# Kernel tuning notes

Measured on AMD Instinct MI355X. Metric: run time of the kernel, lower is better.

Reference implementation:

```python
import jax, jax.numpy as jnp
import numpy as np

B, T, S, D = 32, 1024, 1024, 512
VOCAB = 1000
INSERT_TOK = jnp.array([1, 2], dtype=jnp.int64)


def setup_inputs() -> dict:
    key = jax.random.key(0)
    k1, k2, k3, k4, k5 = jax.random.split(key, 5)
    input_var = jax.random.randint(k1, (B, T), 0, VOCAB, dtype=jnp.int64)
    output = jax.random.normal(k2, (B, T, D), jnp.float32)
    context = jax.random.normal(k3, (B, S, D), jnp.float32)
    # nn.Linear(2*dim, dim): weight [D, 2D], bias [D]
    W = jax.random.normal(k4, (D, 2 * D), jnp.float32) / np.sqrt(2 * D)
    b = jax.random.normal(k5, (D,), jnp.float32) * 0.01
    return {"input_var": input_var, "output": output, "context": context,
            "di": 0, "W": W, "b": b}


def _hard_align(input_var, src_len):
    """Replicates the python double-loop: sequential 'inserted' counter per batch.
    Returns (j, valid): j[b,i] = column of the 1.0 in attn row i (torch negative
    indices wrapped), valid[b,i] = whether row i gets any 1.0 at all."""
    bsz, tgt_len = input_var.shape
    flags = jnp.isin(input_var, INSERT_TOK)  # [B,T] is token an insert token

    def step(inserted, xi):
        i, flag = xi  # i: scalar position, flag: [B]
        cond = (src_len >= i - inserted)                    # gate, per batch
        ins2 = inserted + jnp.where(cond & flag, 1, 0)      # increment before write
        j = i - ins2 - 1
        j = jnp.where(j < 0, j + src_len, j)                # torch negative-index wrap
        return ins2, (j, cond)

    idxs = jnp.arange(1, tgt_len, dtype=jnp.int32)
    init = jnp.zeros((bsz,), jnp.int32)  # init_inserted()
    _, (j_rows, valid) = jax.lax.scan(step, init, (idxs, flags[:, 1:].T))
    j_rows = j_rows.T      # [B,T-1]
    valid = valid.T        # [B,T-1]
    # row 0: attn[b,0,0] = 1.0 always
    j_full = jnp.concatenate([jnp.zeros((bsz, 1), j_rows.dtype), j_rows], axis=1)
    valid_full = jnp.concatenate([jnp.ones((bsz, 1), bool), valid], axis=1)
    return j_full, valid_full


def reference(input_var, output, context, di, W, b):
    bsz, tgt_len, hid = output.shape
    src_len = context.shape[1]
    j, valid = _hard_align(input_var, src_len)              # [B,T], [B,T]
    vf = valid[:, :, None].astype(output.dtype)
    # hard one-hot attention matrix (as the module materializes it)
    attn = jax.nn.one_hot(j, src_len, dtype=output.dtype) * vf  # [B,T,S]
    # mix = bmm(attn, context) == masked gather of context rows
    mix = jnp.take_along_axis(context, j[:, :, None].astype(jnp.int32), axis=1) * vf
    combined = jnp.concatenate([mix, output], axis=-1)      # [B,T,2D]
    out = jnp.tanh(combined @ W.T + b)                      # [B,T,D]
    return out, attn
```

## Files before the change

kernel.cpp:

```cpp
#include <hip/hip_runtime.h>
#include <hip/hip_bf16.h>

#define B_ 32
#define T_ 1024
#define S_ 1024
#define D_ 512
#define M_ (B_*T_)
#define N_ D_
#define K_ (2*D_)

typedef __attribute__((ext_vector_type(8))) short bf16x8;
typedef __attribute__((ext_vector_type(4))) float f32x4;

__device__ inline unsigned short f2bf(float x) {
    union { float f; unsigned u; } v; v.f = x;
    unsigned r = v.u + 0x7FFFu + ((v.u >> 16) & 1u);
    return (unsigned short)(r >> 16);
}

__device__ inline unsigned cvt2bf(float lo, float hi) {
#if __has_builtin(__builtin_amdgcn_cvt_pk_bf16_f32)
    typedef __attribute__((ext_vector_type(2))) __bf16 bf2;
    union { bf2 v; unsigned u; } r;
    r.v = __builtin_amdgcn_cvt_pk_bf16_f32(lo, hi);
    return r.u;
#else
    return (unsigned)f2bf(lo) | ((unsigned)f2bf(hi) << 16);
#endif
}

__device__ inline float fast_tanh(float x) {
#if __has_builtin(__builtin_amdgcn_exp2f) && __has_builtin(__builtin_amdgcn_rcpf)
    const float e = __builtin_amdgcn_exp2f(x * 2.885390082f);
    const float r = __builtin_amdgcn_rcpf(e + 1.0f);
    return 1.0f - 2.0f * r;
#else
    return tanhf(x);
#endif
}

__global__ void align_kernel(const int* __restrict__ iv, int* __restrict__ jbuf) {
    const int b = blockIdx.x;
    const int lane = threadIdx.x;
    const int* row = iv + b * T_;
    int f[16];
    int local = 0;
    const int t0 = lane * 16;
    #pragma unroll
    for (int q = 0; q < 16; ++q) {
        const int t = t0 + q;
        const int tok = row[t];
        const int fl = (t > 0 && (tok == 1 || tok == 2)) ? 1 : 0;
        f[q] = fl;
        local += fl;
    }
    int incl = local;
    #pragma unroll
    for (int off = 1; off < 64; off <<= 1) {
        const int up = __shfl_up(incl, off, 64);
        if (lane >= off) incl += up;
    }
    int run = incl - local;
    #pragma unroll
    for (int q = 0; q < 16; ++q) {
        const int t = t0 + q;
        run += f[q];
        int j;
        if (t == 0) {
            j = 0;
        } else {
            j = t - run - 1;
            if (j < 0) j += S_;
        }
        jbuf[b * T_ + t] = j;
    }
}

__global__ void pack_w(const float* __restrict__ W, unsigned short* __restrict__ Wbf) {
    const int idx = blockIdx.x * blockDim.x + threadIdx.x;
    const f32x4 a = ((const f32x4*)W)[idx * 2];
    const f32x4 c = ((const f32x4*)W)[idx * 2 + 1];
    union { bf16x8 v; unsigned u[4]; } pk;
    pk.u[0] = cvt2bf(a[0], a[1]); pk.u[1] = cvt2bf(a[2], a[3]);
    pk.u[2] = cvt2bf(c[0], c[1]); pk.u[3] = cvt2bf(c[2], c[3]);
    *(bf16x8*)(Wbf + (size_t)idx * 8) = pk.v;
}

#define BM 128
#define BN 128
#define BK 64
#define KMAX (K_ - BK)
#define NGEMM ((M_ / BM) * (N_ / BN))
#define NATTN 512

__global__ __launch_bounds__(256, 3)
void gemm_attn(const unsigned short* __restrict__ Wbf,
               const float* __restrict__ bias,
               float* __restrict__ out,
               float* __restrict__ attn,
               const float* __restrict__ ctx,
               const float* __restrict__ outp,
               const int* __restrict__ jbuf) {
    const int bx = blockIdx.x;
    const int tid = threadIdx.x;

    if (bx < NATTN) {
        const int m0 = bx * 64;
        #pragma unroll 4
        for (int r = 0; r < 64; ++r) {
            const int row = m0 + r;
            const int j = jbuf[row];
            f32x4 v = {0.f, 0.f, 0.f, 0.f};
            if ((j >> 2) == tid) v[j & 3] = 1.0f;
            ((f32x4*)(attn + (size_t)row * S_))[tid] = v;
        }
        return;
    }

    __shared__ unsigned short As[BM * BK];
    __shared__ unsigned short Bs[BN * BK];

    const int gbx  = bx - NATTN;
    const int lane = tid & 63;
    const int wave = tid >> 6;
    const int wm = wave >> 1, wn = wave & 1;
    const int l16 = lane & 15, quad = lane >> 4;

    const int xcd = gbx & 7;
    const int bn  = (gbx >> 3) & 3;
    const int bm  = ((gbx >> 5) << 3) | xcd;
    const int mBase = bm * BM;
    const int nBase = bn * BN;

    const int kc   = tid & 7;
    const int rsub = tid >> 3;
    const int sw   = kc ^ (rsub & 7);
    const float* actx[4];
    const float* aout[4];
    #pragma unroll
    for (int it = 0; it < 4; ++it) {
        const int r = it * 32 + rsub;
        const int m = mBase + r;
        const int jm = jbuf[m];
        actx[it] = ctx + ((size_t)((m >> 10) * S_ + jm)) * D_ + kc * 8;
        aout[it] = outp + (size_t)m * D_ - D_ + kc * 8;
    }

    f32x4 acc[4][4] = {};
    f32x4 fa[4][2];

#define LOAD_A(KO) do {                                                        \
    const int _koa = (KO);                                                     \
    _Pragma("unroll")                                                          \
    for (int _it = 0; _it < 4; ++_it) {                                        \
        const float* _src = (_koa < D_) ? (actx[_it] + _koa) : (aout[_it] + _koa); \
        fa[_it][0] = ((const f32x4*)_src)[0];                                  \
        fa[_it][1] = ((const f32x4*)_src)[1];                                  \
    }                                                                          \
} while (0)

    LOAD_A(0);

    for (int ko = 0; ko < K_; ko += BK) {
        #pragma unroll
        for (int it = 0; it < 4; ++it) {
            const int chunk = it * 256 + tid;
            const int row = chunk >> 3;
            const int kcb = chunk & 7;
            const int gk8 = (kcb ^ (row & 7)) * 8;
            const unsigned short* gB = Wbf + (size_t)(nBase + row) * K_ + ko + gk8;
            __builtin_amdgcn_global_load_lds(
                (const __attribute__((address_space(1))) void*)gB,
                (__attribute__((address_space(3))) void*)(Bs + chunk * 8), 16, 0, 0);
        }
        #pragma unroll
        for (int it = 0; it < 4; ++it) {
            union { bf16x8 v; unsigned u[4]; } pk;
            pk.u[0] = cvt2bf(fa[it][0][0], fa[it][0][1]);
            pk.u[1] = cvt2bf(fa[it][0][2], fa[it][0][3]);
            pk.u[2] = cvt2bf(fa[it][1][0], fa[it][1][1]);
            pk.u[3] = cvt2bf(fa[it][1][2], fa[it][1][3]);
            *(bf16x8*)&As[(it * 256 + rsub * 8 + sw) * 8] = pk.v;
        }
        __syncthreads();

        {
            const int ko2 = (ko + BK > KMAX) ? KMAX : ko + BK;
            LOAD_A(ko2);
        }

        #pragma unroll
        for (int ks = 0; ks < 2; ++ks) {
            bf16x8 af[4], bfr[4];
            #pragma unroll
            for (int mt = 0; mt < 4; ++mt) {
                const int r = wm * 64 + mt * 16 + l16;
                const int q = ks * 4 + quad;
                af[mt] = *(const bf16x8*)&As[(r * 8 + (q ^ (r & 7))) * 8];
            }
            #pragma unroll
            for (int nt = 0; nt < 4; ++nt) {
                const int r = wn * 64 + nt * 16 + l16;
                const int q = ks * 4 + quad;
                bfr[nt] = *(const bf16x8*)&Bs[(r * 8 + (q ^ (r & 7))) * 8];
            }
            #pragma unroll
            for (int mt = 0; mt < 4; ++mt)
                #pragma unroll
                for (int nt = 0; nt < 4; ++nt)
                    acc[mt][nt] = __builtin_amdgcn_mfma_f32_16x16x32_bf16(
                        af[mt], bfr[nt], acc[mt][nt], 0, 0, 0);
        }
        __syncthreads();
    }

#undef LOAD_A

    #pragma unroll
    for (int nt = 0; nt < 4; ++nt) {
        const int n = nBase + wn * 64 + nt * 16 + l16;
        const float bv = bias[n];
        #pragma unroll
        for (int mt = 0; mt < 4; ++mt) {
            #pragma unroll
            for (int r = 0; r < 4; ++r) {
                const int m = mBase + wm * 64 + mt * 16 + quad * 4 + r;
                out[(size_t)m * N_ + n] = fast_tanh(acc[mt][nt][r] + bv);
            }
        }
    }
}

extern "C" void kernel_launch(void* const* d_in, const int* in_sizes, int n_in,
                              void* d_out, int out_size, void* d_ws, size_t ws_size,
                              hipStream_t stream) {
    const int*   iv   = (const int*)d_in[0];
    const float* outp = (const float*)d_in[1];
    const float* ctx  = (const float*)d_in[2];
    const float* W    = (const float*)d_in[4];
    const float* bias = (const float*)d_in[5];

    float* out  = (float*)d_out;
    float* attn = out + (size_t)M_ * N_;

    int* jbuf = (int*)d_ws;
    unsigned short* Wbf = (unsigned short*)((char*)d_ws + (size_t)M_ * 4);

    align_kernel<<<B_, 64, 0, stream>>>(iv, jbuf);
    pack_w<<<(N_ * K_ / 8) / 256, 256, 0, stream>>>(W, Wbf);
    gemm_attn<<<NGEMM + NATTN, 256, 0, stream>>>(Wbf, bias, out, attn, ctx, outp, jbuf);
}
```

Before: 336.0 us.

## Enlarge GEMM tiles to 256x256 with 512-thread blocks

Doubles the GEMM block tile in both M and N, moving to 8 waves per block where each wave computes a 64x128 sub-tile. The goal is more data reuse per LDS load and fewer GEMM blocks, so the grid fills the CUs in roughly a single pass. The attention one-hot writer blocks now sit after the GEMM blocks, and the W source pointers are computed once before the K loop. In exchange, LDS use doubles to 64KB per block and each thread holds 128 accumulator floats, which under the 2-blocks-per-CU launch bound risks register pressure or spills and lowers occupancy.

```diff
diff --git a/kernel.cpp b/kernel.cpp
--- a/kernel.cpp
+++ b/kernel.cpp
@@ -86,14 +86,14 @@
     *(bf16x8*)(Wbf + (size_t)idx * 8) = pk.v;
 }
 
-#define BM 128
-#define BN 128
+#define BM 256
+#define BN 256
 #define BK 64
 #define KMAX (K_ - BK)
 #define NGEMM ((M_ / BM) * (N_ / BN))
 #define NATTN 512
 
-__global__ __launch_bounds__(256, 3)
+__global__ __launch_bounds__(512, 2)
 void gemm_attn(const unsigned short* __restrict__ Wbf,
                const float* __restrict__ bias,
                float* __restrict__ out,
@@ -104,49 +104,52 @@
     const int bx = blockIdx.x;
     const int tid = threadIdx.x;
 
-    if (bx < NATTN) {
-        const int m0 = bx * 64;
+    __shared__ unsigned short As[BM * BK];
+    __shared__ unsigned short Bs[BN * BK];
+
+    if (bx >= NGEMM) {
+        const int m0 = (bx - NGEMM) * 64;
+        const int col  = tid & 255;
+        const int half = tid >> 8;
         #pragma unroll 4
-        for (int r = 0; r < 64; ++r) {
-            const int row = m0 + r;
+        for (int r = 0; r < 32; ++r) {
+            const int row = m0 + r * 2 + half;
             const int j = jbuf[row];
             f32x4 v = {0.f, 0.f, 0.f, 0.f};
-            if ((j >> 2) == tid) v[j & 3] = 1.0f;
-            ((f32x4*)(attn + (size_t)row * S_))[tid] = v;
+            if ((j >> 2) == col) v[j & 3] = 1.0f;
+            ((f32x4*)(attn + (size_t)row * S_))[col] = v;
         }
         return;
     }
 
-    __shared__ unsigned short As[BM * BK];
-    __shared__ unsigned short Bs[BN * BK];
-
-    const int gbx  = bx - NATTN;
     const int lane = tid & 63;
     const int wave = tid >> 6;
     const int wm = wave >> 1, wn = wave & 1;
     const int l16 = lane & 15, quad = lane >> 4;
 
-    const int xcd = gbx & 7;
-    const int bn  = (gbx >> 3) & 3;
-    const int bm  = ((gbx >> 5) << 3) | xcd;
+    const int xcd = bx & 7;
+    const int bn  = (bx >> 3) & 1;
+    const int bm  = ((bx >> 4) << 3) | xcd;
     const int mBase = bm * BM;
     const int nBase = bn * BN;
 
-    const int kc   = tid & 7;
+    const int g    = tid & 7;
     const int rsub = tid >> 3;
-    const int sw   = kc ^ (rsub & 7);
+    const int sw   = g ^ (rsub & 7);
     const float* actx[4];
     const float* aout[4];
+    const unsigned short* bSrc[4];
     #pragma unroll
     for (int it = 0; it < 4; ++it) {
-        const int r = it * 32 + rsub;
+        const int r = it * 64 + rsub;
         const int m = mBase + r;
         const int jm = jbuf[m];
-        actx[it] = ctx + ((size_t)((m >> 10) * S_ + jm)) * D_ + kc * 8;
-        aout[it] = outp + (size_t)m * D_ - D_ + kc * 8;
-    }
-
-    f32x4 acc[4][4] = {};
+        actx[it] = ctx + ((size_t)((m >> 10) * S_ + jm)) * D_ + g * 8;
+        aout[it] = outp + (size_t)m * D_ - D_ + g * 8;
+        bSrc[it] = Wbf + (size_t)(nBase + r) * K_ + sw * 8;
+    }
+
+    f32x4 acc[4][8] = {};
     f32x4 fa[4][2];
 
 #define LOAD_A(KO) do {                                                        \
@@ -164,14 +167,10 @@
     for (int ko = 0; ko < K_; ko += BK) {
         #pragma unroll
         for (int it = 0; it < 4; ++it) {
-            const int chunk = it * 256 + tid;
-            const int row = chunk >> 3;
-            const int kcb = chunk & 7;
-            const int gk8 = (kcb ^ (row & 7)) * 8;
-            const unsigned short* gB = Wbf + (size_t)(nBase + row) * K_ + ko + gk8;
             __builtin_amdgcn_global_load_lds(
-                (const __attribute__((address_space(1))) void*)gB,
-                (__attribute__((address_space(3))) void*)(Bs + chunk * 8), 16, 0, 0);
+                (const __attribute__((address_space(1))) void*)(bSrc[it] + ko),
+                (__attribute__((address_space(3))) void*)(Bs + (it * 512 + tid) * 8),
+                16, 0, 0);
         }
         #pragma unroll
         for (int it = 0; it < 4; ++it) {
@@ -180,7 +179,7 @@
             pk.u[1] = cvt2bf(fa[it][0][2], fa[it][0][3]);
             pk.u[2] = cvt2bf(fa[it][1][0], fa[it][1][1]);
             pk.u[3] = cvt2bf(fa[it][1][2], fa[it][1][3]);
-            *(bf16x8*)&As[(it * 256 + rsub * 8 + sw) * 8] = pk.v;
+            *(bf16x8*)&As[(it * 512 + rsub * 8 + sw) * 8] = pk.v;
         }
         __syncthreads();
 
@@ -191,23 +190,22 @@
 
         #pragma unroll
         for (int ks = 0; ks < 2; ++ks) {
-            bf16x8 af[4], bfr[4];
+            bf16x8 af[4], bfr[8];
+            const int q = ks * 4 + quad;
             #pragma unroll
             for (int mt = 0; mt < 4; ++mt) {
                 const int r = wm * 64 + mt * 16 + l16;
-                const int q = ks * 4 + quad;
                 af[mt] = *(const bf16x8*)&As[(r * 8 + (q ^ (r & 7))) * 8];
             }
             #pragma unroll
-            for (int nt = 0; nt < 4; ++nt) {
-                const int r = wn * 64 + nt * 16 + l16;
-                const int q = ks * 4 + quad;
-                bfr[nt] = *(const bf16x8*)&Bs[(r * 8 + (q ^ (r & 7))) * 8];
+            for (int nt = 0; nt < 8; ++nt) {
+                const int rb = wn * 128 + nt * 16 + l16;
+                bfr[nt] = *(const bf16x8*)&Bs[(rb * 8 + (q ^ (rb & 7))) * 8];
             }
             #pragma unroll
             for (int mt = 0; mt < 4; ++mt)
                 #pragma unroll
-                for (int nt = 0; nt < 4; ++nt)
+                for (int nt = 0; nt < 8; ++nt)
                     acc[mt][nt] = __builtin_amdgcn_mfma_f32_16x16x32_bf16(
                         af[mt], bfr[nt], acc[mt][nt], 0, 0, 0);
         }
@@ -217,8 +215,8 @@
 #undef LOAD_A
 
     #pragma unroll
-    for (int nt = 0; nt < 4; ++nt) {
-        const int n = nBase + wn * 64 + nt * 16 + l16;
+    for (int nt = 0; nt < 8; ++nt) {
+        const int n = nBase + wn * 128 + nt * 16 + l16;
         const float bv = bias[n];
         #pragma unroll
         for (int mt = 0; mt < 4; ++mt) {
@@ -248,5 +246,5 @@
 
     align_kernel<<<B_, 64, 0, stream>>>(iv, jbuf);
     pack_w<<<(N_ * K_ / 8) / 256, 256, 0, stream>>>(W, Wbf);
-    gemm_attn<<<NGEMM + NATTN, 256, 0, stream>>>(Wbf, bias, out, attn, ctx, outp, jbuf);
-}
+    gemm_attn<<<NGEMM + NATTN, 512, 0, stream>>>(Wbf, bias, out, attn, ctx, outp, jbuf);
+}
```

Result: no change. 329.9 us (-1.8%).
